# Kernel tuning notes

Hardware: AMD Instinct MI355X
Metric: run time of the kernel (lower is better)

## Reference

```python
import jax, jax.numpy as jnp
import numpy as np
from jax import lax

M, T, D, E, NTAGS = 512, 512, 128, 512, 74
GH = D // 2   # GRU hidden per direction (64)
LH = E // 2   # LSTM hidden per direction (256)


def _gru_dir(x, Wih, Whh, bih, bhh):
    # x: [T, Din] -> [T, H]; PyTorch gate order r, z, n
    h = Whh.shape[1]
    gi = x @ Wih.T + bih  # [T, 3H] precomputed input projections
    def step(hprev, gi_t):
        gh = hprev @ Whh.T + bhh
        r = jax.nn.sigmoid(gi_t[:h] + gh[:h])
        z = jax.nn.sigmoid(gi_t[h:2 * h] + gh[h:2 * h])
        n = jnp.tanh(gi_t[2 * h:] + r * gh[2 * h:])
        hnew = (1.0 - z) * n + z * hprev
        return hnew, hnew
    _, hs = lax.scan(step, jnp.zeros((h,), x.dtype), gi)
    return hs


def _bigru(x, Wf, Uf, bf, cf, Wb, Ub, bb, cb):
    hf = _gru_dir(x, Wf, Uf, bf, cf)
    hb = _gru_dir(x[::-1], Wb, Ub, bb, cb)[::-1]
    return jnp.concatenate([hf, hb], axis=-1)


def _lstm_dir(x, Wih, Whh, bih, bhh):
    # PyTorch gate order i, f, g, o
    h = Whh.shape[1]
    gi = x @ Wih.T + bih  # [T, 4H]
    def step(carry, gi_t):
        hprev, cprev = carry
        g = gi_t + hprev @ Whh.T + bhh
        i = jax.nn.sigmoid(g[:h])
        f = jax.nn.sigmoid(g[h:2 * h])
        gg = jnp.tanh(g[2 * h:3 * h])
        o = jax.nn.sigmoid(g[3 * h:])
        c = f * cprev + i * gg
        hnew = o * jnp.tanh(c)
        return (hnew, c), hnew
    init = (jnp.zeros((h,), x.dtype), jnp.zeros((h,), x.dtype))
    _, hs = lax.scan(step, init, gi)
    return hs


def _bilstm(x, Wf, Uf, bf, cf, Wb, Ub, bb, cb):
    hf = _lstm_dir(x, Wf, Uf, bf, cf)
    hb = _lstm_dir(x[::-1], Wb, Ub, bb, cb)[::-1]
    return jnp.concatenate([hf, hb], axis=-1)


def setup_inputs() -> dict:
    key = jax.random.key(0)
    ks = jax.random.split(key, 32)
    s = 0.05
    def n(k, shape, scale=s):
        return jax.random.normal(k, shape, jnp.float32) * scale
    inp = {
        'memory': jax.random.normal(ks[0], (M, T, D), jnp.float32),
        'u': jax.random.normal(ks[1], (T, D), jnp.float32),
        'embed': jax.random.normal(ks[2], (T, E), jnp.float32),
        'W_ff': n(ks[3], (D, 2 * D)), 'b_ff': n(ks[4], (D,)),
        'gWih_f': n(ks[5], (3 * GH, D)), 'gWhh_f': n(ks[6], (3 * GH, GH)),
        'gbih_f': n(ks[7], (3 * GH,)), 'gbhh_f': n(ks[8], (3 * GH,)),
        'gWih_b': n(ks[9], (3 * GH, D)), 'gWhh_b': n(ks[10], (3 * GH, GH)),
        'gbih_b': n(ks[11], (3 * GH,)), 'gbhh_b': n(ks[12], (3 * GH,)),
        'W_k': n(ks[13], (E, D)), 'b_k': n(ks[14], (E,)),
        'lWih_f': n(ks[15], (4 * LH, E)), 'lWhh_f': n(ks[16], (4 * LH, LH)),
        'lbih_f': n(ks[17], (4 * LH,)), 'lbhh_f': n(ks[18], (4 * LH,)),
        'lWih_b': n(ks[19], (4 * LH, E)), 'lWhh_b': n(ks[20], (4 * LH, LH)),
        'lbih_b': n(ks[21], (4 * LH,)), 'lbhh_b': n(ks[22], (4 * LH,)),
        'W_out': n(ks[23], (NTAGS, E)), 'b_out': n(ks[24], (NTAGS,)),
    }
    return inp


def reference(memory, u, embed, W_ff, b_ff,
              gWih_f, gWhh_f, gbih_f, gbhh_f,
              gWih_b, gWhh_b, gbih_b, gbhh_b,
              W_k, b_k,
              lWih_f, lWhh_f, lbih_f, lbhh_f,
              lWih_b, lWhh_b, lbih_b, lbhh_b,
              W_out, b_out):
    # --- memory attention (original: python loop over self._memory) ---
    # p[i] = <flatten(memory[i]), flatten(u)>; softmax over memories
    p = jax.nn.softmax(jnp.einsum('mtd,td->m', memory, u))  # [M]
    cat = jnp.concatenate([memory, jnp.broadcast_to(u, memory.shape)], axis=-1)  # [M,T,2D]
    g = cat @ W_ff.T + b_ff  # [M,T,D] (ff_layer applied per memory)
    G = jnp.einsum('m,mtd->td', p, g)  # weighted sum over memories [T,D]
    # --- session encoder (bidirectional GRU) ---
    h = _bigru(G, gWih_f, gWhh_f, gbih_f, gbhh_f, gWib := gWih_b, gWhh_b, gbih_b, gbhh_b)  # [T,D]
    # --- knowledge encoder ---
    o = (u + h) @ W_k.T + b_k  # [T,E]
    # --- tagging head: BiLSTM over embed + o, then linear + softmax ---
    x = embed + o
    comb = _bilstm(x, lWih_f, lWhh_f, lbih_f, lbhh_f, lWih_b, lWhh_b, lbih_b, lbhh_b)  # [T,E]
    logits = comb @ W_out.T + b_out  # [T, NTAGS]
    return jax.nn.softmax(logits, axis=-1)
```

## Files before the change

### kernel.cpp

```cpp
#include <hip/hip_runtime.h>
#include <math.h>

#define TT 512
#define DD 128
#define MM 512
#define EE 512
#define NTAGS 74
#define GH 64
#define LH 256

typedef _Float16 half_t;
typedef _Float16 v2h __attribute__((ext_vector_type(2)));
typedef _Float16 v8h __attribute__((ext_vector_type(8)));
typedef _Float16 v16h __attribute__((ext_vector_type(16)));
typedef int v4i __attribute__((ext_vector_type(4)));

__device__ __forceinline__ float fdot2f(v2h a, v2h b, float c) {
#if __has_builtin(__builtin_amdgcn_fdot2)
    return __builtin_amdgcn_fdot2(a, b, c, false);
#else
    return c + (float)a[0] * (float)b[0] + (float)a[1] * (float)b[1];
#endif
}

__device__ __forceinline__ int sdot4(int a, int b, int c) {
#if __has_builtin(__builtin_amdgcn_sdot4)
    return __builtin_amdgcn_sdot4(a, b, c, false);
#else
    return c + ((a << 24) >> 24) * ((b << 24) >> 24)
             + ((a << 16) >> 24) * ((b << 16) >> 24)
             + ((a << 8) >> 24) * ((b << 8) >> 24)
             + (a >> 24) * (b >> 24);
#endif
}

__device__ __forceinline__ float sigf(float x) { return 1.f / (1.f + __expf(-x)); }
__device__ __forceinline__ float tanhfast(float x) { return 1.f - 2.f / (__expf(2.f * x) + 1.f); }

__device__ __forceinline__ void lds_barrier() {
    asm volatile("s_waitcnt lgkmcnt(0)" ::: "memory");
    __builtin_amdgcn_s_barrier();
}

__device__ __forceinline__ int preduce_i(int x) {
    x += __builtin_amdgcn_mov_dpp(x, 0xB1, 0xF, 0xF, true);
    return x;
}
__device__ __forceinline__ float qreduce_f(float x) {
    x += __int_as_float(__builtin_amdgcn_mov_dpp(__float_as_int(x), 0xB1, 0xF, 0xF, true));
    x += __int_as_float(__builtin_amdgcn_mov_dpp(__float_as_int(x), 0x4E, 0xF, 0xF, true));
    return x;
}

__device__ __forceinline__ v16h load16(const float* p) {
    float4 x0 = ((const float4*)p)[0];
    float4 x1 = ((const float4*)p)[1];
    float4 x2 = ((const float4*)p)[2];
    float4 x3 = ((const float4*)p)[3];
    v16h r;
    r[0] = (half_t)x0.x; r[1] = (half_t)x0.y; r[2] = (half_t)x0.z; r[3] = (half_t)x0.w;
    r[4] = (half_t)x1.x; r[5] = (half_t)x1.y; r[6] = (half_t)x1.z; r[7] = (half_t)x1.w;
    r[8] = (half_t)x2.x; r[9] = (half_t)x2.y; r[10] = (half_t)x2.z; r[11] = (half_t)x2.w;
    r[12] = (half_t)x3.x; r[13] = (half_t)x3.y; r[14] = (half_t)x3.z; r[15] = (half_t)x3.w;
    return r;
}

#define OPAQUE3(a, b, c) asm volatile("" : "+v"(a), "+v"(b), "+v"(c))
#define OPAQUE4(a, b, c, d) asm volatile("" : "+v"(a), "+v"(b), "+v"(c), "+v"(d))

__device__ __forceinline__ void dot16(const v16h& w, const v8h& h0, const v8h& h1,
                                      float& x0, float& x1) {
    x0 = fdot2f(v2h{w[0], w[1]}, v2h{h0[0], h0[1]}, x0);
    x1 = fdot2f(v2h{w[2], w[3]}, v2h{h0[2], h0[3]}, x1);
    x0 = fdot2f(v2h{w[4], w[5]}, v2h{h0[4], h0[5]}, x0);
    x1 = fdot2f(v2h{w[6], w[7]}, v2h{h0[6], h0[7]}, x1);
    x0 = fdot2f(v2h{w[8], w[9]}, v2h{h1[0], h1[1]}, x0);
    x1 = fdot2f(v2h{w[10], w[11]}, v2h{h1[2], h1[3]}, x1);
    x0 = fdot2f(v2h{w[12], w[13]}, v2h{h1[4], h1[5]}, x0);
    x1 = fdot2f(v2h{w[14], w[15]}, v2h{h1[6], h1[7]}, x1);
}

__device__ __forceinline__ int pack4(int b0, int b1, int b2, int b3) {
    return (b0 & 0xff) | ((b1 & 0xff) << 8) | ((b2 & 0xff) << 16) | (b3 << 24);
}

__device__ __forceinline__ v4i quant16(const float* p, float inv_s) {
    float4 x0 = ((const float4*)p)[0];
    float4 x1 = ((const float4*)p)[1];
    float4 x2 = ((const float4*)p)[2];
    float4 x3 = ((const float4*)p)[3];
    v4i r;
    r.x = pack4(__float2int_rn(x0.x * inv_s), __float2int_rn(x0.y * inv_s),
                __float2int_rn(x0.z * inv_s), __float2int_rn(x0.w * inv_s));
    r.y = pack4(__float2int_rn(x1.x * inv_s), __float2int_rn(x1.y * inv_s),
                __float2int_rn(x1.z * inv_s), __float2int_rn(x1.w * inv_s));
    r.z = pack4(__float2int_rn(x2.x * inv_s), __float2int_rn(x2.y * inv_s),
                __float2int_rn(x2.z * inv_s), __float2int_rn(x2.w * inv_s));
    r.w = pack4(__float2int_rn(x3.x * inv_s), __float2int_rn(x3.y * inv_s),
                __float2int_rn(x3.z * inv_s), __float2int_rn(x3.w * inv_s));
    return r;
}

__device__ __forceinline__ float rowmax128(const float* p) {
    float m = 0.f;
#pragma unroll 8
    for (int k = 0; k < 128; k += 4) {
        float4 a = *(const float4*)(p + k);
        m = fmaxf(m, fmaxf(fmaxf(fabsf(a.x), fabsf(a.y)), fmaxf(fabsf(a.z), fabsf(a.w))));
    }
    return m;
}

__global__ __launch_bounds__(256) void k_dots(const float* __restrict__ mem,
                                              const float* __restrict__ u,
                                              float* __restrict__ dots) {
    int m = blockIdx.x;
    const float4* m4 = (const float4*)(mem + (size_t)m * TT * DD);
    const float4* u4 = (const float4*)u;
    float acc = 0.f;
#pragma unroll 4
    for (int it = 0; it < (TT * DD / 4) / 256; ++it) {
        int i = it * 256 + threadIdx.x;
        float4 a = m4[i], b = u4[i];
        acc += a.x * b.x + a.y * b.y + a.z * b.z + a.w * b.w;
    }
    for (int off = 32; off; off >>= 1) acc += __shfl_down(acc, off, 64);
    __shared__ float red[4];
    int w = threadIdx.x >> 6, l = threadIdx.x & 63;
    if (l == 0) red[w] = acc;
    __syncthreads();
    if (threadIdx.x == 0) dots[m] = red[0] + red[1] + red[2] + red[3];
}

__global__ __launch_bounds__(512) void k_softmax_p(const float* __restrict__ dots,
                                                   float* __restrict__ p) {
    int tid = threadIdx.x;
    float v = dots[tid];
    float mx = v;
    for (int off = 32; off; off >>= 1) mx = fmaxf(mx, __shfl_down(mx, off, 64));
    __shared__ float red[8];
    __shared__ float bm, bs;
    int w = tid >> 6, l = tid & 63;
    if (l == 0) red[w] = mx;
    __syncthreads();
    if (tid == 0) {
        float t = red[0];
        for (int i = 1; i < 8; ++i) t = fmaxf(t, red[i]);
        bm = t;
    }
    __syncthreads();
    float e = __expf(v - bm);
    float sm = e;
    for (int off = 32; off; off >>= 1) sm += __shfl_down(sm, off, 64);
    if (l == 0) red[w] = sm;
    __syncthreads();
    if (tid == 0) {
        float t = 0.f;
        for (int i = 0; i < 8; ++i) t += red[i];
        bs = t;
    }
    __syncthreads();
    p[tid] = e / bs;
}

__global__ __launch_bounds__(128) void k_wsum(const float* __restrict__ mem,
                                              const float* __restrict__ p,
                                              float* __restrict__ Mbar) {
    __shared__ float pl[MM];
    for (int i = threadIdx.x; i < MM; i += 128) pl[i] = p[i];
    __syncthreads();
    int i4 = blockIdx.x * 128 + threadIdx.x;
    const float4* m4 = (const float4*)mem;
    float4 acc = {0.f, 0.f, 0.f, 0.f};
#pragma unroll 4
    for (int m = 0; m < MM; ++m) {
        float pm = pl[m];
        float4 a = m4[(size_t)m * (TT * DD / 4) + i4];
        acc.x += pm * a.x; acc.y += pm * a.y; acc.z += pm * a.z; acc.w += pm * a.w;
    }
    ((float4*)Mbar)[i4] = acc;
}

__global__ __launch_bounds__(128) void k_G(const float* __restrict__ Mbar,
                                           const float* __restrict__ u,
                                           const float* __restrict__ Wff,
                                           const float* __restrict__ bff,
                                           float* __restrict__ G) {
    int t = blockIdx.x, d = threadIdx.x;
    __shared__ __align__(16) float Ml[DD], ul[DD];
    Ml[d] = Mbar[t * DD + d];
    ul[d] = u[t * DD + d];
    __syncthreads();
    const float* wr = Wff + (size_t)d * 2 * DD;
    float a0 = 0.f, a1 = 0.f;
#pragma unroll 4
    for (int k = 0; k < DD; ++k) {
        a0 += Ml[k] * wr[k];
        a1 += ul[k] * wr[DD + k];
    }
    G[t * DD + d] = a0 + a1 + bff[d];
}

__global__ __launch_bounds__(384) void k_gru_gi(const float* __restrict__ G,
                                                const float* __restrict__ Wf,
                                                const float* __restrict__ bf,
                                                const float* __restrict__ Wb,
                                                const float* __restrict__ bb,
                                                float* __restrict__ gi) {
    int t = blockIdx.x;
    __shared__ __align__(16) float Gl[DD];
    if (threadIdx.x < DD) Gl[threadIdx.x] = G[t * DD + threadIdx.x];
    __syncthreads();
    int r = threadIdx.x;
    int dir = r >= 192;
    int rr = dir ? r - 192 : r;
    int gate = rr >> 6, unit = rr & 63;
    const float* w = (dir ? Wb : Wf) + (size_t)rr * DD;
    float b = (dir ? bb : bf)[rr];
    float a0 = 0.f, a1 = 0.f;
#pragma unroll 4
    for (int k = 0; k < DD; k += 2) {
        a0 += Gl[k] * w[k];
        a1 += Gl[k + 1] * w[k + 1];
    }
    gi[((size_t)dir * TT + t) * 256 + unit * 4 + gate] = a0 + a1 + b;
}

__global__ __launch_bounds__(256) void k_gru_seq(const float* __restrict__ Whh_f,
                                                 const float* __restrict__ bhh_f,
                                                 const float* __restrict__ Whh_b,
                                                 const float* __restrict__ bhh_b,
                                                 const float* __restrict__ gi,
                                                 float* __restrict__ hbufT) {
    int dir = blockIdx.x;
    int tid = threadIdx.x;
    int u = tid >> 2;
    int q = tid & 3;
    const float* Whh = dir ? Whh_b : Whh_f;
    const float* bhh = dir ? bhh_b : bhh_f;
    v16h wr = load16(Whh + (size_t)u * 64 + q * 16);
    v16h wz = load16(Whh + (size_t)(64 + u) * 64 + q * 16);
    v16h wn = load16(Whh + (size_t)(128 + u) * 64 + q * 16);
    OPAQUE3(wr, wz, wn);
    float bh_r = bhh[u], bh_z = bhh[64 + u], bh_n = bhh[128 + u];

    const float* gbase = gi + (size_t)dir * TT * 256 + u * 4;

    __shared__ __align__(16) half_t hl[2][64];
    if (tid < 64) hl[0][tid] = (half_t)0.f;
    float h = 0.f;
    float4 gq0, gq1, gq2, gq3;
#define GPRO(J) { \
    int tp_ = dir ? (TT - 1 - (J)) : (J); \
    gq##J = *(const float4*)(gbase + (size_t)tp_ * 256); }
    GPRO(0); GPRO(1); GPRO(2); GPRO(3);
#undef GPRO
    lds_barrier();

    float hs0 = 0.f, hs1 = 0.f, hs2 = 0.f, hs3 = 0.f;
#define GSTEP(J, HS) { \
    int s_ = s4 + (J); \
    const v8h* hv_ = (const v8h*)&hl[s_ & 1][q * 16]; \
    v8h h0_ = hv_[0], h1_ = hv_[1]; \
    float ar0 = 0.f, ar1 = 0.f, az0 = 0.f, az1 = 0.f, an0 = 0.f, an1 = 0.f; \
    dot16(wr, h0_, h1_, ar0, ar1); \
    dot16(wz, h0_, h1_, az0, az1); \
    dot16(wn, h0_, h1_, an0, an1); \
    float srd = qreduce_f(ar0 + ar1); \
    float szd = qreduce_f(az0 + az1); \
    float snd = qreduce_f(an0 + an1); \
    float r_ = sigf(gq##J.x + srd + bh_r); \
    float z_ = sigf(gq##J.y + szd + bh_z); \
    float n_ = tanhfast(gq##J.z + r_ * (snd + bh_n)); \
    h = (1.f - z_) * n_ + z_ * h; \
    if (q == 0) hl[(s_ + 1) & 1][u] = (half_t)h; \
    HS = h; \
    int sp_ = s_ + 4; if (sp_ >= TT) sp_ = TT - 1; \
    int tp_ = dir ? (TT - 1 - sp_) : sp_; \
    gq##J = *(const float4*)(gbase + (size_t)tp_ * 256); \
    lds_barrier(); }

    for (int s4 = 0; s4 < TT; s4 += 4) {
        GSTEP(0, hs0);
        GSTEP(1, hs1);
        GSTEP(2, hs2);
        GSTEP(3, hs3);
        if (q == 0) {
            float4 v;
            int tb;
            if (dir == 0) { tb = s4; v = {hs0, hs1, hs2, hs3}; }
            else          { tb = TT - 4 - s4; v = {hs3, hs2, hs1, hs0}; }
            *(float4*)(hbufT + (size_t)(dir * 64 + u) * TT + tb) = v;
        }
    }
#undef GSTEP
}

__global__ __launch_bounds__(512) void k_x(const float* __restrict__ u,
                                           const float* __restrict__ hbufT,
                                           const float* __restrict__ Wk,
                                           const float* __restrict__ bk,
                                           const float* __restrict__ embed,
                                           float* __restrict__ x) {
    int t = blockIdx.x, e = threadIdx.x;
    __shared__ __align__(16) float sl[DD];
    if (e < DD) sl[e] = u[t * DD + e] + hbufT[(size_t)e * TT + t];
    __syncthreads();
    const float* wr = Wk + (size_t)e * DD;
    float a0 = 0.f, a1 = 0.f;
#pragma unroll 4
    for (int k = 0; k < DD; k += 2) {
        a0 += sl[k] * wr[k];
        a1 += sl[k + 1] * wr[k + 1];
    }
    x[t * EE + e] = embed[t * EE + e] + a0 + a1 + bk[e];
}

__global__ __launch_bounds__(1024) void k_lstm_gi(const float* __restrict__ x,
                                                  const float* __restrict__ Wf,
                                                  const float* __restrict__ bf,
                                                  const float* __restrict__ Wb,
                                                  const float* __restrict__ bb,
                                                  float* __restrict__ gi) {
    int dir = blockIdx.y;
    int t0 = blockIdx.x * 8;
    __shared__ __align__(16) float xl[8 * EE];
    for (int i = threadIdx.x; i < 8 * EE; i += 1024) xl[i] = x[(size_t)t0 * EE + i];
    __syncthreads();
    int r = threadIdx.x;
    int gate = r >> 8, un = r & 255;
    const float* W = dir ? Wb : Wf;
    const float* bi = dir ? bb : bf;
    const float* wr = W + (size_t)r * EE;
    float b = bi[r];
    float acc[8];
#pragma unroll
    for (int uu = 0; uu < 8; ++uu) acc[uu] = b;
    for (int k = 0; k < EE; k += 4) {
        float4 wv = *(const float4*)(wr + k);
#pragma unroll
        for (int uu = 0; uu < 8; ++uu) {
            float4 xv = *(const float4*)(&xl[uu * EE + k]);
            acc[uu] += wv.x * xv.x + wv.y * xv.y + wv.z * xv.z + wv.w * xv.w;
        }
    }
#pragma unroll
    for (int uu = 0; uu < 8; ++uu)
        gi[((size_t)dir * TT + (t0 + uu)) * 1024 + un * 4 + gate] = acc[uu];
}

__global__ __launch_bounds__(512) __attribute__((amdgpu_waves_per_eu(2, 2)))
void k_lstm_seq(const float* __restrict__ Whh_f,
                const float* __restrict__ bhh_f,
                const float* __restrict__ Whh_b,
                const float* __restrict__ bhh_b,
                const float* __restrict__ gi,
                float* __restrict__ combT) {
    int dir = blockIdx.x;
    int tid = threadIdx.x;
    int u = tid >> 1;
    int half = tid & 1;
    const float* Whh = dir ? Whh_b : Whh_f;
    const float* bhh = dir ? bhh_b : bhh_f;

    __shared__ __align__(16) int hq[2][64];

    const float* ri = Whh + (size_t)u * 256 + half * 128;
    const float* rf = ri + 256 * 256;
    const float* rg = ri + 512 * 256;
    const float* ro = ri + 768 * 256;

    float mi = rowmax128(ri); mi = fmaxf(mi, __shfl_xor(mi, 1, 64));
    float mf = rowmax128(rf); mf = fmaxf(mf, __shfl_xor(mf, 1, 64));
    float mg = rowmax128(rg); mg = fmaxf(mg, __shfl_xor(mg, 1, 64));
    float mo = rowmax128(ro); mo = fmaxf(mo, __shfl_xor(mo, 1, 64));
    float fs_i = mi / 16129.f, fs_f = mf / 16129.f, fs_g = mg / 16129.f, fs_o = mo / 16129.f;

    float inv_i = 127.f / mi, inv_f = 127.f / mf, inv_g = 127.f / mg, inv_o = 127.f / mo;
#define DECLG(P, ptr, inv)                                                        \
    v4i P##0 = quant16((ptr), (inv)),       P##1 = quant16((ptr) + 16, (inv)),    \
        P##2 = quant16((ptr) + 32, (inv)),  P##3 = quant16((ptr) + 48, (inv)),    \
        P##4 = quant16((ptr) + 64, (inv)),  P##5 = quant16((ptr) + 80, (inv)),    \
        P##6 = quant16((ptr) + 96, (inv)),  P##7 = quant16((ptr) + 112, (inv));   \
    OPAQUE4(P##0, P##1, P##2, P##3);                                              \
    OPAQUE4(P##4, P##5, P##6, P##7)

    DECLG(wi, ri, inv_i);
    DECLG(wf, rf, inv_f);
    DECLG(wg, rg, inv_g);
    DECLG(wo, ro, inv_o);
#undef DECLG

    float bh_i = bhh[u], bh_f = bhh[256 + u], bh_g = bhh[512 + u], bh_o = bhh[768 + u];
    if (tid < 64) hq[0][tid] = 0;
    float c_state = 0.f;

    const float* gbase = gi + (size_t)dir * TT * 1024 + u * 4;

    float4 gq0, gq1, gq2, gq3;
#define LPRO(J) { \
    int tp_ = dir ? (TT - 1 - (J)) : (J); \
    gq##J = *(const float4*)(gbase + (size_t)tp_ * 1024); }
    LPRO(0); LPRO(1); LPRO(2); LPRO(3);
#undef LPRO
    lds_barrier();

    float hs0 = 0.f, hs1 = 0.f, hs2 = 0.f, hs3 = 0.f;
#define LD1(P, C, HV, A0, A1) \
    A0 = sdot4((P##C).x, HV.x, A0); A1 = sdot4((P##C).y, HV.y, A1); \
    A0 = sdot4((P##C).z, HV.z, A0); A1 = sdot4((P##C).w, HV.w, A1)
#define LDOT8(P, A0, A1) \
    LD1(P, 0, h0_, A0, A1); LD1(P, 1, h1_, A0, A1); \
    LD1(P, 2, h2_, A0, A1); LD1(P, 3, h3_, A0, A1); \
    LD1(P, 4, h4_, A0, A1); LD1(P, 5, h5_, A0, A1); \
    LD1(P, 6, h6_, A0, A1); LD1(P, 7, h7_, A0, A1)

#define LSTEP(J, HS) { \
    int s_ = s4 + (J); \
    const v4i* hb_ = (const v4i*)&hq[s_ & 1][half * 32]; \
    v4i h0_ = hb_[0], h1_ = hb_[1], h2_ = hb_[2], h3_ = hb_[3]; \
    v4i h4_ = hb_[4], h5_ = hb_[5], h6_ = hb_[6], h7_ = hb_[7]; \
    int ai0 = 0, ai1 = 0, af0 = 0, af1 = 0, ag0 = 0, ag1 = 0, ao0 = 0, ao1 = 0; \
    LDOT8(wi, ai0, ai1); \
    LDOT8(wf, af0, af1); \
    LDOT8(wg, ag0, ag1); \
    LDOT8(wo, ao0, ao1); \
    int ai_ = preduce_i(ai0 + ai1); \
    int af_ = preduce_i(af0 + af1); \
    int ag_ = preduce_i(ag0 + ag1); \
    int ao_ = preduce_i(ao0 + ao1); \
    float iv = sigf((float)ai_ * fs_i + bh_i + gq##J.x); \
    float fv = sigf((float)af_ * fs_f + bh_f + gq##J.y); \
    float gv = tanhfast((float)ag_ * fs_g + bh_g + gq##J.z); \
    float ov = sigf((float)ao_ * fs_o + bh_o + gq##J.w); \
    c_state = fv * c_state + iv * gv; \
    HS = ov * tanhfast(c_state); \
    if (half == 0) ((signed char*)hq[(s_ + 1) & 1])[u] = (signed char)__float2int_rn(HS * 127.f); \
    int sp_ = s_ + 4; if (sp_ >= TT) sp_ = TT - 1; \
    int tp_ = dir ? (TT - 1 - sp_) : sp_; \
    gq##J = *(const float4*)(gbase + (size_t)tp_ * 1024); \
    lds_barrier(); }

    for (int s4 = 0; s4 < TT; s4 += 4) {
        LSTEP(0, hs0);
        LSTEP(1, hs1);
        LSTEP(2, hs2);
        LSTEP(3, hs3);
        if (half == 0) {
            float4 v;
            int tb;
            if (dir == 0) { tb = s4; v = {hs0, hs1, hs2, hs3}; }
            else          { tb = TT - 4 - s4; v = {hs3, hs2, hs1, hs0}; }
            *(float4*)(combT + (size_t)(dir * 256 + u) * TT + tb) = v;
        }
    }
#undef LSTEP
#undef LDOT8
#undef LD1
}

__global__ __launch_bounds__(128) void k_out(const float* __restrict__ combT,
                                             const float* __restrict__ Wout,
                                             const float* __restrict__ bout,
                                             float* __restrict__ out) {
    int t = blockIdx.x;
    __shared__ __align__(16) float cl[EE];
    __shared__ float ll[NTAGS];
    __shared__ float mred, sred;
    for (int i = threadIdx.x; i < EE; i += 128) cl[i] = combT[(size_t)i * TT + t];
    __syncthreads();
    int e = threadIdx.x;
    if (e < NTAGS) {
        const float* wr = Wout + (size_t)e * EE;
        float a0 = 0.f, a1 = 0.f;
#pragma unroll 4
        for (int k = 0; k < EE; k += 2) {
            a0 += cl[k] * wr[k];
            a1 += cl[k + 1] * wr[k + 1];
        }
        ll[e] = a0 + a1 + bout[e];
    }
    __syncthreads();
    if (threadIdx.x == 0) {
        float m = ll[0];
        for (int i = 1; i < NTAGS; ++i) m = fmaxf(m, ll[i]);
        float ss = 0.f;
        for (int i = 0; i < NTAGS; ++i) ss += __expf(ll[i] - m);
        mred = m;
        sred = ss;
    }
    __syncthreads();
    if (e < NTAGS) out[t * NTAGS + e] = __expf(ll[e] - mred) / sred;
}

#define OFF_DOTS  ((size_t)0)
#define OFF_P     ((size_t)512)
#define OFF_MBAR  ((size_t)1024)
#define OFF_G     ((size_t)66560)
#define OFF_HBUF  ((size_t)328704)
#define OFF_X     ((size_t)394240)
#define OFF_GIL   ((size_t)656384)
#define OFF_COMB  ((size_t)1704960)
#define OFF_GIG   OFF_COMB

extern "C" void kernel_launch(void* const* d_in, const int* in_sizes, int n_in,
                              void* d_out, int out_size, void* d_ws, size_t ws_size,
                              hipStream_t stream) {
    const float* memory = (const float*)d_in[0];
    const float* u      = (const float*)d_in[1];
    const float* embed  = (const float*)d_in[2];
    const float* W_ff   = (const float*)d_in[3];
    const float* b_ff   = (const float*)d_in[4];
    const float* gWih_f = (const float*)d_in[5];
    const float* gWhh_f = (const float*)d_in[6];
    const float* gbih_f = (const float*)d_in[7];
    const float* gbhh_f = (const float*)d_in[8];
    const float* gWih_b = (const float*)d_in[9];
    const float* gWhh_b = (const float*)d_in[10];
    const float* gbih_b = (const float*)d_in[11];
    const float* gbhh_b = (const float*)d_in[12];
    const float* W_k    = (const float*)d_in[13];
    const float* b_k    = (const float*)d_in[14];
    const float* lWih_f = (const float*)d_in[15];
    const float* lWhh_f = (const float*)d_in[16];
    const float* lbih_f = (const float*)d_in[17];
    const float* lbhh_f = (const float*)d_in[18];
    const float* lWih_b = (const float*)d_in[19];
    const float* lWhh_b = (const float*)d_in[20];
    const float* lbih_b = (const float*)d_in[21];
    const float* lbhh_b = (const float*)d_in[22];
    const float* W_out  = (const float*)d_in[23];
    const float* b_out  = (const float*)d_in[24];
    float* out = (float*)d_out;
    float* ws = (float*)d_ws;

    float* dots  = ws + OFF_DOTS;
    float* p     = ws + OFF_P;
    float* Mbar  = ws + OFF_MBAR;
    float* G     = ws + OFF_G;
    float* giG   = ws + OFF_GIG;
    float* hbufT = ws + OFF_HBUF;
    float* x     = ws + OFF_X;
    float* giL   = ws + OFF_GIL;
    float* combT = ws + OFF_COMB;

    k_dots<<<MM, 256, 0, stream>>>(memory, u, dots);
    k_softmax_p<<<1, MM, 0, stream>>>(dots, p);
    k_wsum<<<128, 128, 0, stream>>>(memory, p, Mbar);
    k_G<<<TT, DD, 0, stream>>>(Mbar, u, W_ff, b_ff, G);
    k_gru_gi<<<TT, 384, 0, stream>>>(G, gWih_f, gbih_f, gWih_b, gbih_b, giG);
    k_gru_seq<<<2, 256, 0, stream>>>(gWhh_f, gbhh_f, gWhh_b, gbhh_b, giG, hbufT);
    k_x<<<TT, EE, 0, stream>>>(u, hbufT, W_k, b_k, embed, x);
    k_lstm_gi<<<dim3(64, 2), 1024, 0, stream>>>(x, lWih_f, lbih_f, lWih_b, lbih_b, giL);
    k_lstm_seq<<<2, 512, 0, stream>>>(lWhh_f, lbhh_f, lWhh_b, lbhh_b, giL, combT);
    k_out<<<TT, 128, 0, stream>>>(combT, W_out, b_out, out);
}
```

Baseline: 1.157 ms.

## Stage recurrent gate inputs into LDS via async global-to-LDS double buffering

The GRU and LSTM sequential kernels now prefetch 8 timesteps of precomputed input projections at a time. They use global_load_lds directly into a double-buffered shared buffer and wait on vmcnt only once per 8-step chunk. Before, each step issued its own per-thread float4 global load for step s+4. The goal is to take global-memory latency and per-step vmcnt waits off the serial recurrence's critical path. The cost is extra LDS use (64 KB for the LSTM buffer), and output stores now go through address-space-qualified pointers.

Result: slower. 1.184 ms (+2.4%).

```diff
diff --git a/kernel.cpp b/kernel.cpp
--- a/kernel.cpp
+++ b/kernel.cpp
@@ -14,6 +14,7 @@
 typedef _Float16 v8h __attribute__((ext_vector_type(8)));
 typedef _Float16 v16h __attribute__((ext_vector_type(16)));
 typedef int v4i __attribute__((ext_vector_type(4)));
+typedef float vf4 __attribute__((ext_vector_type(4)));
 
 __device__ __forceinline__ float fdot2f(v2h a, v2h b, float c) {
 #if __has_builtin(__builtin_amdgcn_fdot2)
@@ -40,6 +41,21 @@
 __device__ __forceinline__ void lds_barrier() {
     asm volatile("s_waitcnt lgkmcnt(0)" ::: "memory");
     __builtin_amdgcn_s_barrier();
+}
+__device__ __forceinline__ void wait_vmcnt0() {
+    asm volatile("s_waitcnt vmcnt(0)" ::: "memory");
+}
+
+typedef const __attribute__((address_space(1))) void* as1cv;
+typedef __attribute__((address_space(3))) void* as3v;
+__device__ __forceinline__ void gload_lds16(const float* g, float* l) {
+    __builtin_amdgcn_global_load_lds((as1cv)g, (as3v)l, 16, 0, 0);
+}
+
+typedef __attribute__((address_space(1))) vf4 g4_t;
+__device__ __forceinline__ void gstore4(float* p, float a, float b, float c, float d) {
+    vf4 v = {a, b, c, d};
+    *(g4_t*)p = v;
 }
 
 __device__ __forceinline__ int preduce_i(int x) {
@@ -244,23 +260,27 @@
     OPAQUE3(wr, wz, wn);
     float bh_r = bhh[u], bh_z = bhh[64 + u], bh_n = bhh[128 + u];
 
-    const float* gbase = gi + (size_t)dir * TT * 256 + u * 4;
-
+    const float* gdir = gi + (size_t)dir * TT * 256;
+
+    __shared__ __align__(16) float gbuf[2][8][256];
     __shared__ __align__(16) half_t hl[2][64];
+
+#define GSTAGE(C, B) { \
+    int tb_ = dir ? (TT - 8 * ((C) + 1)) : (8 * (C)); \
+    const float* gs_ = gdir + (size_t)tb_ * 256; \
+    gload_lds16(gs_ + (tid) * 4, &gbuf[B][0][0] + (tid) * 4); \
+    gload_lds16(gs_ + (256 + tid) * 4, &gbuf[B][0][0] + (256 + tid) * 4); }
+
+    GSTAGE(0, 0);
     if (tid < 64) hl[0][tid] = (half_t)0.f;
     float h = 0.f;
-    float4 gq0, gq1, gq2, gq3;
-#define GPRO(J) { \
-    int tp_ = dir ? (TT - 1 - (J)) : (J); \
-    gq##J = *(const float4*)(gbase + (size_t)tp_ * 256); }
-    GPRO(0); GPRO(1); GPRO(2); GPRO(3);
-#undef GPRO
+    wait_vmcnt0();
     lds_barrier();
 
     float hs0 = 0.f, hs1 = 0.f, hs2 = 0.f, hs3 = 0.f;
 #define GSTEP(J, HS) { \
-    int s_ = s4 + (J); \
-    const v8h* hv_ = (const v8h*)&hl[s_ & 1][q * 16]; \
+    float4 gq = *(const float4*)&gbuf[buf][dir ? 7 - (J) : (J)][u * 4]; \
+    const v8h* hv_ = (const v8h*)&hl[(J) & 1][q * 16]; \
     v8h h0_ = hv_[0], h1_ = hv_[1]; \
     float ar0 = 0.f, ar1 = 0.f, az0 = 0.f, az1 = 0.f, an0 = 0.f, an1 = 0.f; \
     dot16(wr, h0_, h1_, ar0, ar1); \
@@ -269,31 +289,31 @@
     float srd = qreduce_f(ar0 + ar1); \
     float szd = qreduce_f(az0 + az1); \
     float snd = qreduce_f(an0 + an1); \
-    float r_ = sigf(gq##J.x + srd + bh_r); \
-    float z_ = sigf(gq##J.y + szd + bh_z); \
-    float n_ = tanhfast(gq##J.z + r_ * (snd + bh_n)); \
+    float r_ = sigf(gq.x + srd + bh_r); \
+    float z_ = sigf(gq.y + szd + bh_z); \
+    float n_ = tanhfast(gq.z + r_ * (snd + bh_n)); \
     h = (1.f - z_) * n_ + z_ * h; \
-    if (q == 0) hl[(s_ + 1) & 1][u] = (half_t)h; \
+    if (q == 0) hl[((J) + 1) & 1][u] = (half_t)h; \
     HS = h; \
-    int sp_ = s_ + 4; if (sp_ >= TT) sp_ = TT - 1; \
-    int tp_ = dir ? (TT - 1 - sp_) : sp_; \
-    gq##J = *(const float4*)(gbase + (size_t)tp_ * 256); \
+    if ((J) == 7) wait_vmcnt0(); \
     lds_barrier(); }
 
-    for (int s4 = 0; s4 < TT; s4 += 4) {
-        GSTEP(0, hs0);
-        GSTEP(1, hs1);
-        GSTEP(2, hs2);
-        GSTEP(3, hs3);
-        if (q == 0) {
-            float4 v;
-            int tb;
-            if (dir == 0) { tb = s4; v = {hs0, hs1, hs2, hs3}; }
-            else          { tb = TT - 4 - s4; v = {hs3, hs2, hs1, hs0}; }
-            *(float4*)(hbufT + (size_t)(dir * 64 + u) * TT + tb) = v;
-        }
+#define GSTORE(S4) { \
+    if (q == 0) { \
+        if (dir == 0) gstore4(hbufT + (size_t)(dir * 64 + u) * TT + (S4), hs0, hs1, hs2, hs3); \
+        else          gstore4(hbufT + (size_t)(dir * 64 + u) * TT + (TT - 4 - (S4)), hs3, hs2, hs1, hs0); } }
+
+    for (int c = 0; c < TT / 8; ++c) {
+        int buf = c & 1;
+        if (c + 1 < TT / 8) GSTAGE(c + 1, buf ^ 1);
+        GSTEP(0, hs0); GSTEP(1, hs1); GSTEP(2, hs2); GSTEP(3, hs3);
+        GSTORE(8 * c);
+        GSTEP(4, hs0); GSTEP(5, hs1); GSTEP(6, hs2); GSTEP(7, hs3);
+        GSTORE(8 * c + 4);
     }
 #undef GSTEP
+#undef GSTORE
+#undef GSTAGE
 }
 
 __global__ __launch_bounds__(512) void k_x(const float* __restrict__ u,
@@ -363,6 +383,7 @@
     const float* Whh = dir ? Whh_b : Whh_f;
     const float* bhh = dir ? bhh_b : bhh_f;
 
+    __shared__ __align__(16) float gbuf[2][8][1024];
     __shared__ __align__(16) int hq[2][64];
 
     const float* ri = Whh + (size_t)u * 256 + half * 128;
@@ -392,17 +413,21 @@
 #undef DECLG
 
     float bh_i = bhh[u], bh_f = bhh[256 + u], bh_g = bhh[512 + u], bh_o = bhh[768 + u];
+
+    const float* gdir = gi + (size_t)dir * TT * 1024;
+
+#define LSTAGE(C, B) { \
+    int tb_ = dir ? (TT - 8 * ((C) + 1)) : (8 * (C)); \
+    const float* gs_ = gdir + (size_t)tb_ * 1024; \
+    gload_lds16(gs_ + (tid) * 4, &gbuf[B][0][0] + (tid) * 4); \
+    gload_lds16(gs_ + (512 + tid) * 4, &gbuf[B][0][0] + (512 + tid) * 4); \
+    gload_lds16(gs_ + (1024 + tid) * 4, &gbuf[B][0][0] + (1024 + tid) * 4); \
+    gload_lds16(gs_ + (1536 + tid) * 4, &gbuf[B][0][0] + (1536 + tid) * 4); }
+
+    LSTAGE(0, 0);
     if (tid < 64) hq[0][tid] = 0;
     float c_state = 0.f;
-
-    const float* gbase = gi + (size_t)dir * TT * 1024 + u * 4;
-
-    float4 gq0, gq1, gq2, gq3;
-#define LPRO(J) { \
-    int tp_ = dir ? (TT - 1 - (J)) : (J); \
-    gq##J = *(const float4*)(gbase + (size_t)tp_ * 1024); }
-    LPRO(0); LPRO(1); LPRO(2); LPRO(3);
-#undef LPRO
+    wait_vmcnt0();
     lds_barrier();
 
     float hs0 = 0.f, hs1 = 0.f, hs2 = 0.f, hs3 = 0.f;
@@ -416,8 +441,8 @@
     LD1(P, 6, h6_, A0, A1); LD1(P, 7, h7_, A0, A1)
 
 #define LSTEP(J, HS) { \
-    int s_ = s4 + (J); \
-    const v4i* hb_ = (const v4i*)&hq[s_ & 1][half * 32]; \
+    float4 gq = *(const float4*)&gbuf[buf][dir ? 7 - (J) : (J)][u * 4]; \
+    const v4i* hb_ = (const v4i*)&hq[(J) & 1][half * 32]; \
     v4i h0_ = hb_[0], h1_ = hb_[1], h2_ = hb_[2], h3_ = hb_[3]; \
     v4i h4_ = hb_[4], h5_ = hb_[5], h6_ = hb_[6], h7_ = hb_[7]; \
     int ai0 = 0, ai1 = 0, af0 = 0, af1 = 0, ag0 = 0, ag1 = 0, ao0 = 0, ao1 = 0; \
@@ -429,32 +454,32 @@
     int af_ = preduce_i(af0 + af1); \
     int ag_ = preduce_i(ag0 + ag1); \
     int ao_ = preduce_i(ao0 + ao1); \
-    float iv = sigf((float)ai_ * fs_i + bh_i + gq##J.x); \
-    float fv = sigf((float)af_ * fs_f + bh_f + gq##J.y); \
-    float gv = tanhfast((float)ag_ * fs_g + bh_g + gq##J.z); \
-    float ov = sigf((float)ao_ * fs_o + bh_o + gq##J.w); \
+    float iv = sigf((float)ai_ * fs_i + bh_i + gq.x); \
+    float fv = sigf((float)af_ * fs_f + bh_f + gq.y); \
+    float gv = tanhfast((float)ag_ * fs_g + bh_g + gq.z); \
+    float ov = sigf((float)ao_ * fs_o + bh_o + gq.w); \
     c_state = fv * c_state + iv * gv; \
     HS = ov * tanhfast(c_state); \
-    if (half == 0) ((signed char*)hq[(s_ + 1) & 1])[u] = (signed char)__float2int_rn(HS * 127.f); \
-    int sp_ = s_ + 4; if (sp_ >= TT) sp_ = TT - 1; \
-    int tp_ = dir ? (TT - 1 - sp_) : sp_; \
-    gq##J = *(const float4*)(gbase + (size_t)tp_ * 1024); \
+    if (half == 0) ((signed char*)hq[((J) + 1) & 1])[u] = (signed char)__float2int_rn(HS * 127.f); \
+    if ((J) == 7) wait_vmcnt0(); \
     lds_barrier(); }
 
-    for (int s4 = 0; s4 < TT; s4 += 4) {
-        LSTEP(0, hs0);
-        LSTEP(1, hs1);
-        LSTEP(2, hs2);
-        LSTEP(3, hs3);
-        if (half == 0) {
-            float4 v;
-            int tb;
-            if (dir == 0) { tb = s4; v = {hs0, hs1, hs2, hs3}; }
-            else          { tb = TT - 4 - s4; v = {hs3, hs2, hs1, hs0}; }
-            *(float4*)(combT + (size_t)(dir * 256 + u) * TT + tb) = v;
-        }
+#define LSTORE(S4) { \
+    if (half == 0) { \
+        if (dir == 0) gstore4(combT + (size_t)(dir * 256 + u) * TT + (S4), hs0, hs1, hs2, hs3); \
+        else          gstore4(combT + (size_t)(dir * 256 + u) * TT + (TT - 4 - (S4)), hs3, hs2, hs1, hs0); } }
+
+    for (int c = 0; c < TT / 8; ++c) {
+        int buf = c & 1;
+        if (c + 1 < TT / 8) LSTAGE(c + 1, buf ^ 1);
+        LSTEP(0, hs0); LSTEP(1, hs1); LSTEP(2, hs2); LSTEP(3, hs3);
+        LSTORE(8 * c);
+        LSTEP(4, hs0); LSTEP(5, hs1); LSTEP(6, hs2); LSTEP(7, hs3);
+        LSTORE(8 * c + 4);
     }
 #undef LSTEP
+#undef LSTORE
+#undef LSTAGE
 #undef LDOT8
 #undef LD1
 }
```
